# Kernel optimization log

Hardware: AMD Instinct MI355X
Metric: run time of the kernel (lower is better)

The kernel has to match this reference:

```python
import jax, jax.numpy as jnp
import numpy as np

# Multi-scale deformable attention (MSDeformableAttention from RTDETRTransformerv2)
SPATIAL = ((80, 80), (40, 40), (20, 20))  # (h, w) per level, strides 8/16/32 on 640x640
N_HEADS, N_LEVELS, N_POINTS = 8, 3, 4
D_MODEL = 256
HEAD_DIM = D_MODEL // N_HEADS


def setup_inputs() -> dict:
    key = jax.random.key(0)
    ks = jax.random.split(key, 10)
    B, Q = 16, 300
    Lv = sum(h * w for h, w in SPATIAL)  # 8400
    s = 0.02
    return {
        "query": jax.random.normal(ks[0], (B, Q, D_MODEL), jnp.float32),
        "reference_points": jax.random.uniform(ks[1], (B, Q, 4), jnp.float32),
        "value": jax.random.normal(ks[2], (B, Lv, D_MODEL), jnp.float32),
        "Wv": jax.random.normal(ks[3], (D_MODEL, D_MODEL), jnp.float32) * s,
        "bv": jnp.zeros((D_MODEL,), jnp.float32),
        "Woff": jax.random.normal(ks[4], (D_MODEL, N_HEADS * N_LEVELS * N_POINTS * 2), jnp.float32) * s,
        "boff": jax.random.normal(ks[5], (N_HEADS * N_LEVELS * N_POINTS * 2,), jnp.float32) * 0.1,
        "Wattn": jax.random.normal(ks[6], (D_MODEL, N_HEADS * N_LEVELS * N_POINTS), jnp.float32) * s,
        "battn": jnp.zeros((N_HEADS * N_LEVELS * N_POINTS,), jnp.float32),
        "Wout": jax.random.normal(ks[7], (D_MODEL, D_MODEL), jnp.float32) * s,
        "bout": jnp.zeros((D_MODEL,), jnp.float32),
    }


def _grid_sample_level(v_lvl, gx, gy, h, w):
    """Bilinear grid_sample, align_corners=False, zeros padding.

    v_lvl : (B, nH, h*w, hd) flattened per-level value map
    gx,gy : (B, nH, P) sample coords in [-1, 1]
    returns (B, nH, P, hd)
    """
    px = ((gx + 1.0) * w - 1.0) * 0.5  # pixel x
    py = ((gy + 1.0) * h - 1.0) * 0.5  # pixel y
    x0 = jnp.floor(px)
    y0 = jnp.floor(py)
    fx = px - x0
    fy = py - y0
    x0i = x0.astype(jnp.int32)
    y0i = y0.astype(jnp.int32)

    def corner(xi, yi, wgt):
        valid = (xi >= 0) & (xi < w) & (yi >= 0) & (yi < h)
        idx = jnp.clip(yi, 0, h - 1) * w + jnp.clip(xi, 0, w - 1)
        g = jnp.take_along_axis(v_lvl, idx[..., None], axis=2)  # (B,nH,P,hd)
        return g * (wgt * valid.astype(wgt.dtype))[..., None]

    return (corner(x0i, y0i, (1 - fx) * (1 - fy))
            + corner(x0i + 1, y0i, fx * (1 - fy))
            + corner(x0i, y0i + 1, (1 - fx) * fy)
            + corner(x0i + 1, y0i + 1, fx * fy))


def reference(query, reference_points, value, Wv, bv, Woff, boff, Wattn, battn, Wout, bout):
    B, Q, _ = query.shape
    # value projection -> per-head values
    v = (value @ Wv + bv).reshape(B, -1, N_HEADS, HEAD_DIM)
    # sampling offsets and attention weights from queries
    off = (query @ Woff + boff).reshape(B, Q, N_HEADS, N_LEVELS, N_POINTS, 2)
    aw = jax.nn.softmax(
        (query @ Wattn + battn).reshape(B, Q, N_HEADS, N_LEVELS * N_POINTS), axis=-1
    ).reshape(B, Q, N_HEADS, N_LEVELS, N_POINTS)
    # reference points (cx, cy) broadcast over heads/levels/points
    ref = reference_points[:, :, None, None, None, :2]
    pts = jnp.clip(ref + off, 0.0, 1.0)      # (B,Q,nH,nL,nP,2) in [0,1]
    g = pts * 2.0 - 1.0                      # grid_sample coords in [-1,1]

    out = jnp.zeros((B, Q, N_HEADS, HEAD_DIM), query.dtype)
    start = 0
    for lvl, (h, w) in enumerate(SPATIAL):
        v_lvl = v[:, start:start + h * w].transpose(0, 2, 1, 3)  # (B,nH,hw,hd)
        gl = g[:, :, :, lvl]                                     # (B,Q,nH,nP,2)
        gx = gl[..., 0].transpose(0, 2, 1, 3).reshape(B, N_HEADS, Q * N_POINTS)
        gy = gl[..., 1].transpose(0, 2, 1, 3).reshape(B, N_HEADS, Q * N_POINTS)
        sampled = _grid_sample_level(v_lvl, gx, gy, h, w)        # (B,nH,Q*nP,hd)
        sampled = sampled.reshape(B, N_HEADS, Q, N_POINTS, HEAD_DIM)
        wl = aw[:, :, :, lvl].transpose(0, 2, 1, 3)              # (B,nH,Q,nP)
        out = out + jnp.einsum('bhqpd,bhqp->bqhd', sampled, wl)
        start += h * w

    return out.reshape(B, Q, D_MODEL) @ Wout + bout
```

## Files before the change

kernel.cpp:

```cpp
#include <hip/hip_runtime.h>
#include <hip/hip_bf16.h>
#include <cstddef>

#define NB 16
#define NQ 300
#define DM 256
#define LV_ 8400

typedef __attribute__((ext_vector_type(8))) short short8;
typedef __attribute__((ext_vector_type(4))) float f32x4;

static __device__ __forceinline__ unsigned short bf16_rne(float f) {
  unsigned int u = __builtin_bit_cast(unsigned int, f);
  u += 0x7FFFu + ((u >> 16) & 1u);
  return (unsigned short)(u >> 16);
}

static __device__ __forceinline__ unsigned int pack_bf2(float a, float b) {
  __hip_bfloat162 p = __float22bfloat162_rn(make_float2(a, b));
  unsigned int u;
  __builtin_memcpy(&u, &p, 4);
  return u;
}

__global__ __launch_bounds__(256) void prep_kernel(
    const float* __restrict__ Wv, const float* __restrict__ Wout,
    unsigned short* __restrict__ Wth, unsigned short* __restrict__ WoutT) {
  const float* src = blockIdx.z ? Wout : Wv;
  unsigned short* dst = blockIdx.z ? WoutT : Wth;
  __shared__ float tle[32][33];
  const int k0 = blockIdx.x * 32, n0 = blockIdx.y * 32;
  const int xx = threadIdx.x & 31, y4 = (threadIdx.x >> 5) * 4;
  #pragma unroll
  for (int i = 0; i < 4; ++i)
    tle[y4 + i][xx] = src[(size_t)(k0 + y4 + i) * DM + n0 + xx];
  __syncthreads();
  #pragma unroll
  for (int i = 0; i < 4; ++i)
    dst[(size_t)(n0 + y4 + i) * DM + k0 + xx] = bf16_rne(tle[xx][y4 + i]);
}

__global__ __launch_bounds__(256) void vproj_mfma(
    const float* __restrict__ A, const unsigned short* __restrict__ Wth,
    const float* __restrict__ bias, unsigned short* __restrict__ V) {
  __shared__ short Ah[4][128][8];
  __shared__ short Bh[4][128][8];
  const int tid = threadIdx.x;
  const int lane = tid & 63;
  const int wave = tid >> 6;
  const int l16 = lane & 15, q4 = lane >> 4;
  const int wr = (wave >> 1) * 64, wc = (wave & 1) * 64;
  const size_t row0 = (size_t)blockIdx.x * 128;
  const int col0 = blockIdx.y * 128;

  const int arow = tid >> 1;
  const int half = tid & 1;
  const int c0 = half * 2;

  f32x4 acc[4][4];
  #pragma unroll
  for (int i = 0; i < 4; ++i)
    #pragma unroll
    for (int j = 0; j < 4; ++j) acc[i][j] = (f32x4)0.f;

  const float* ap0 = A + (row0 + arow) * DM + half * 16;
  const unsigned short* wp0 = Wth + (size_t)(col0 + arow) * DM + half * 16;

  float4 f0 = *(const float4*)(ap0 + 0);
  float4 f1 = *(const float4*)(ap0 + 4);
  float4 f2 = *(const float4*)(ap0 + 8);
  float4 f3 = *(const float4*)(ap0 + 12);
  uint4 w0 = *(const uint4*)(wp0);
  uint4 w1 = *(const uint4*)(wp0 + 8);

  for (int kk = 0; kk < DM; kk += 32) {
    uint4 p0, p1;
    p0.x = pack_bf2(f0.x, f0.y); p0.y = pack_bf2(f0.z, f0.w);
    p0.z = pack_bf2(f1.x, f1.y); p0.w = pack_bf2(f1.z, f1.w);
    p1.x = pack_bf2(f2.x, f2.y); p1.y = pack_bf2(f2.z, f2.w);
    p1.z = pack_bf2(f3.x, f3.y); p1.w = pack_bf2(f3.z, f3.w);
    uint4 cw0 = w0, cw1 = w1;
    __syncthreads();
    *(uint4*)&Ah[c0][arow][0]     = p0;
    *(uint4*)&Ah[c0 + 1][arow][0] = p1;
    *(uint4*)&Bh[c0][arow][0]     = cw0;
    *(uint4*)&Bh[c0 + 1][arow][0] = cw1;
    __syncthreads();

    if (kk + 32 < DM) {
      f0 = *(const float4*)(ap0 + kk + 32);
      f1 = *(const float4*)(ap0 + kk + 36);
      f2 = *(const float4*)(ap0 + kk + 40);
      f3 = *(const float4*)(ap0 + kk + 44);
      w0 = *(const uint4*)(wp0 + kk + 32);
      w1 = *(const uint4*)(wp0 + kk + 40);
    }

    short8 af[4], bfr[4];
    #pragma unroll
    for (int i = 0; i < 4; ++i)
      af[i] = *(const short8*)&Ah[q4][wr + i * 16 + l16][0];
    #pragma unroll
    for (int j = 0; j < 4; ++j)
      bfr[j] = *(const short8*)&Bh[q4][wc + j * 16 + l16][0];
    #pragma unroll
    for (int i = 0; i < 4; ++i)
      #pragma unroll
      for (int j = 0; j < 4; ++j)
        acc[i][j] = __builtin_amdgcn_mfma_f32_16x16x32_bf16(af[i], bfr[j], acc[i][j], 0, 0, 0);
  }

  #pragma unroll
  for (int i = 0; i < 4; ++i)
    #pragma unroll
    for (int j = 0; j < 4; ++j) {
      const int col = col0 + wc + j * 16 + l16;
      const float bcol = bias[col];
      #pragma unroll
      for (int r = 0; r < 4; ++r) {
        const size_t row = row0 + wr + i * 16 + q4 * 4 + r;
        V[row * DM + col] = bf16_rne(acc[i][j][r] + bcol);
      }
    }
}

__global__ __launch_bounds__(256) void gemm_qp(
    const float* __restrict__ q,
    const float* __restrict__ Woff, const float* __restrict__ boff,
    const float* __restrict__ Wattn, const float* __restrict__ battn,
    float* __restrict__ offb, float* __restrict__ logitb) {
  const int by = blockIdx.y;
  const float* W; const float* bias; float* C; int N, c0;
  if (by < 6) { W = Woff;  bias = boff;  C = offb;   N = 192; c0 = by * 32; }
  else        { W = Wattn; bias = battn; C = logitb; N = 96;  c0 = (by - 6) * 32; }
  const int m0 = blockIdx.x * 32;

  __shared__ float As[32][33];
  __shared__ float Bs[32][33];
  const int tid = threadIdx.x;
  const int ar = tid >> 3, ak = (tid & 7) * 4;
  const int kr = tid >> 3, bc = (tid & 7) * 4;
  const int tx = tid & 15, ty = tid >> 4;

  const float* apt = q + (size_t)(m0 + ar) * DM + ak;
  float4 av = *(const float4*)apt;
  float4 wv = *(const float4*)(W + (size_t)kr * N + c0 + bc);

  float acc[2][2] = {{0.f, 0.f}, {0.f, 0.f}};
  for (int kk = 0; kk < DM; kk += 32) {
    __syncthreads();
    As[ak + 0][ar] = av.x;
    As[ak + 1][ar] = av.y;
    As[ak + 2][ar] = av.z;
    As[ak + 3][ar] = av.w;
    *(float4*)&Bs[kr][bc] = wv;
    __syncthreads();
    if (kk + 32 < DM) {
      av = *(const float4*)(apt + kk + 32);
      wv = *(const float4*)(W + (size_t)(kk + 32 + kr) * N + c0 + bc);
    }
    #pragma unroll
    for (int k = 0; k < 32; ++k) {
      const float2 a2 = *(const float2*)&As[k][ty * 2];
      const float2 b2 = *(const float2*)&Bs[k][tx * 2];
      acc[0][0] = fmaf(a2.x, b2.x, acc[0][0]);
      acc[0][1] = fmaf(a2.x, b2.y, acc[0][1]);
      acc[1][0] = fmaf(a2.y, b2.x, acc[1][0]);
      acc[1][1] = fmaf(a2.y, b2.y, acc[1][1]);
    }
  }
  const float b0 = bias[c0 + tx * 2], b1 = bias[c0 + tx * 2 + 1];
  #pragma unroll
  for (int i = 0; i < 2; ++i) {
    float2 o; o.x = acc[i][0] + b0; o.y = acc[i][1] + b1;
    *(float2*)&C[(size_t)(m0 + ty * 2 + i) * N + c0 + tx * 2] = o;
  }
}

__global__ __launch_bounds__(256) void sample_kernel(
    const float* __restrict__ refp, const unsigned short* __restrict__ v,
    const float* __restrict__ off, const float* __restrict__ logits,
    unsigned short* __restrict__ mid) {
  const int x = blockIdx.x;
  const int c8 = x & 7, kb = x >> 3;
  const int b = c8 + (kb >= 150 ? 8 : 0);
  const int qp = (kb >= 150 ? kb - 150 : kb);
  const int bq0 = b * NQ + qp * 2;
  const int t = threadIdx.x;
  __shared__ float off_sh[2][192];
  __shared__ float aw_sh[2][96];
  __shared__ int   idx_sh[2][96][4];
  __shared__ float wt_sh[2][96][4];
  __shared__ float ref_sh[2][2];

  {
    const float* osrc = off + (size_t)bq0 * 192;
    float* odst = &off_sh[0][0];
    odst[t] = osrc[t];
    if (t < 128) odst[256 + t] = osrc[256 + t];
    const float* lsrc = logits + (size_t)bq0 * 96;
    if (t < 192) (&aw_sh[0][0])[t] = lsrc[t];
    if (t < 4) ref_sh[t >> 1][t & 1] = refp[(bq0 + (t >> 1)) * 4 + (t & 1)];
  }
  __syncthreads();

  if (t < 16) {
    const int q = t >> 3, h = t & 7;
    float* aw = &aw_sh[q][h * 12];
    float m = -1e30f;
    #pragma unroll
    for (int i = 0; i < 12; ++i) m = fmaxf(m, aw[i]);
    float e[12], s = 0.f;
    #pragma unroll
    for (int i = 0; i < 12; ++i) { e[i] = __expf(aw[i] - m); s += e[i]; }
    const float inv = 1.f / s;
    #pragma unroll
    for (int i = 0; i < 12; ++i) aw[i] = e[i] * inv;
  }
  __syncthreads();

  if (t < 192) {
    const int q = t / 96, r = t - q * 96;
    const int h = r / 12, lp = r - h * 12;
    const int l = lp >> 2, p = lp & 3;
    const int LH[3] = {80, 40, 20};
    const int LS[3] = {0, 6400, 8000};
    const int hh = LH[l], ww = LH[l], st = LS[l];
    const int oi = ((h * 3 + l) * 4 + p) * 2;
    const float aw = aw_sh[q][h * 12 + lp];
    const float sx = fminf(fmaxf(ref_sh[q][0] + off_sh[q][oi], 0.f), 1.f);
    const float sy = fminf(fmaxf(ref_sh[q][1] + off_sh[q][oi + 1], 0.f), 1.f);
    const float px = sx * (float)ww - 0.5f;
    const float py = sy * (float)hh - 0.5f;
    const float x0f = floorf(px), y0f = floorf(py);
    const float fx = px - x0f, fy = py - y0f;
    const int x0 = (int)x0f, y0 = (int)y0f;
    const int x1 = x0 + 1, y1 = y0 + 1;
    const bool vx0 = (x0 >= 0) & (x0 < ww), vx1 = (x1 >= 0) & (x1 < ww);
    const bool vy0 = (y0 >= 0) & (y0 < hh), vy1 = (y1 >= 0) & (y1 < hh);
    const int x0c = min(max(x0, 0), ww - 1), x1c = min(max(x1, 0), ww - 1);
    const int y0c = min(max(y0, 0), hh - 1), y1c = min(max(y1, 0), hh - 1);
    idx_sh[q][r][0] = st + y0c * ww + x0c;
    idx_sh[q][r][1] = st + y0c * ww + x1c;
    idx_sh[q][r][2] = st + y1c * ww + x0c;
    idx_sh[q][r][3] = st + y1c * ww + x1c;
    wt_sh[q][r][0] = aw * (1.f - fx) * (1.f - fy) * ((vx0 & vy0) ? 1.f : 0.f);
    wt_sh[q][r][1] = aw * fx * (1.f - fy) * ((vx1 & vy0) ? 1.f : 0.f);
    wt_sh[q][r][2] = aw * (1.f - fx) * fy * ((vx0 & vy1) ? 1.f : 0.f);
    wt_sh[q][r][3] = aw * fx * fy * ((vx1 & vy1) ? 1.f : 0.f);
  }
  __syncthreads();

  const int q = t >> 7, h = (t >> 4) & 7, dp = t & 15;
  const unsigned short* vb = v + (size_t)b * LV_ * DM + h * 32 + dp * 2;
  float ax = 0.f, ay = 0.f;
  #pragma unroll
  for (int r = 0; r < 12; ++r) {
    const int rr = h * 12 + r;
    #pragma unroll
    for (int cc = 0; cc < 4; ++cc) {
      const int id = idx_sh[q][rr][cc];
      const float w = wt_sh[q][rr][cc];
      const unsigned int u = *(const unsigned int*)(vb + (size_t)id * DM);
      ax = fmaf(w, __builtin_bit_cast(float, u << 16), ax);
      ay = fmaf(w, __builtin_bit_cast(float, u & 0xFFFF0000u), ay);
    }
  }
  unsigned short* mp = mid + (size_t)(bq0 + q) * DM + h * 32 + dp * 2;
  *(unsigned int*)mp = pack_bf2(ax, ay);
}

__global__ __launch_bounds__(256) void outp_mfma(
    const unsigned short* __restrict__ midb, const unsigned short* __restrict__ WoutT,
    const float* __restrict__ bias, float* __restrict__ out) {
  __shared__ short Ah[4][64][8];
  __shared__ short Bh[4][64][8];
  const int tid = threadIdx.x;
  const int lane = tid & 63;
  const int wave = tid >> 6;
  const int l16 = lane & 15, q4 = lane >> 4;
  const int wc = wave * 16;
  const int m0 = blockIdx.x * 64, col0 = blockIdx.y * 64;

  const int r = tid >> 2, ch = tid & 3;
  const unsigned short* apt = midb + (size_t)(m0 + r) * DM + ch * 8;
  const unsigned short* wpt = WoutT + (size_t)(col0 + r) * DM + ch * 8;
  uint4 am = *(const uint4*)apt;
  uint4 wm = *(const uint4*)wpt;

  f32x4 acc[4];
  #pragma unroll
  for (int i = 0; i < 4; ++i) acc[i] = (f32x4)0.f;

  for (int kk = 0; kk < DM; kk += 32) {
    __syncthreads();
    *(uint4*)&Ah[ch][r][0] = am;
    *(uint4*)&Bh[ch][r][0] = wm;
    __syncthreads();
    if (kk + 32 < DM) {
      am = *(const uint4*)(apt + kk + 32);
      wm = *(const uint4*)(wpt + kk + 32);
    }
    const short8 bfrag = *(const short8*)&Bh[q4][wc + l16][0];
    #pragma unroll
    for (int i = 0; i < 4; ++i) {
      const short8 af = *(const short8*)&Ah[q4][i * 16 + l16][0];
      acc[i] = __builtin_amdgcn_mfma_f32_16x16x32_bf16(af, bfrag, acc[i], 0, 0, 0);
    }
  }

  const int col = col0 + wc + l16;
  const float bcol = bias[col];
  #pragma unroll
  for (int i = 0; i < 4; ++i)
    #pragma unroll
    for (int rr = 0; rr < 4; ++rr)
      out[(size_t)(m0 + i * 16 + q4 * 4 + rr) * DM + col] = acc[i][rr] + bcol;
}

extern "C" void kernel_launch(void* const* d_in, const int* in_sizes, int n_in,
                              void* d_out, int out_size, void* d_ws, size_t ws_size,
                              hipStream_t stream) {
  (void)in_sizes; (void)n_in; (void)out_size; (void)ws_size;
  const float* query = (const float*)d_in[0];
  const float* refp  = (const float*)d_in[1];
  const float* value = (const float*)d_in[2];
  const float* Wv    = (const float*)d_in[3];
  const float* bv    = (const float*)d_in[4];
  const float* Woff  = (const float*)d_in[5];
  const float* boff  = (const float*)d_in[6];
  const float* Wattn = (const float*)d_in[7];
  const float* battn = (const float*)d_in[8];
  const float* Wout  = (const float*)d_in[9];
  const float* bout  = (const float*)d_in[10];
  float* out = (float*)d_out;

  char* ws = (char*)d_ws;
  unsigned short* v_bf  = (unsigned short*)ws;
  unsigned short* Wth   = (unsigned short*)(ws + 68812800);
  unsigned short* WoutT = (unsigned short*)(ws + 68943872);
  float* offb   = (float*)(ws + 69074944);
  float* logitb = (float*)(ws + 72761344);
  unsigned short* midb = (unsigned short*)(ws + 74604544);

  prep_kernel<<<dim3(8, 8, 2), 256, 0, stream>>>(Wv, Wout, Wth, WoutT);
  gemm_qp<<<dim3(150, 9), 256, 0, stream>>>(query, Woff, boff, Wattn, battn, offb, logitb);
  vproj_mfma<<<dim3((NB * LV_) / 128, 2), 256, 0, stream>>>(value, Wth, bv, v_bf);
  sample_kernel<<<2400, 256, 0, stream>>>(refp, v_bf, offb, logitb, midb);
  outp_mfma<<<dim3(75, 4), 256, 0, stream>>>(midb, WoutT, bout, out);
}
```

Baseline: 295.6 us.

## Stream value projection without LDS and split sampling per query across corners

The value-projection GEMM drops the LDS-staged 128x128 tiled MFMA kernel. Each wave now computes a 16-row strip across all 256 columns, reading the A fragment straight from global memory and pulling bf16 weight fragments from global/L2 each time, with no barriers. The sampling kernel moves from two queries per block to one query per block, doubling the grid. Within each block, two thread halves handle different bilinear corners and combine their partial sums with a cross-lane shuffle. The aim is to remove LDS sync overhead and raise parallelism in the gather, at the cost of redundant weight reads and more blocks.

```diff
diff --git a/kernel.cpp b/kernel.cpp
--- a/kernel.cpp
+++ b/kernel.cpp
@@ -40,88 +40,47 @@
     dst[(size_t)(n0 + y4 + i) * DM + k0 + xx] = bf16_rne(tle[xx][y4 + i]);
 }
 
-__global__ __launch_bounds__(256) void vproj_mfma(
+__global__ __launch_bounds__(256, 2) void vproj_stream(
     const float* __restrict__ A, const unsigned short* __restrict__ Wth,
     const float* __restrict__ bias, unsigned short* __restrict__ V) {
-  __shared__ short Ah[4][128][8];
-  __shared__ short Bh[4][128][8];
   const int tid = threadIdx.x;
   const int lane = tid & 63;
   const int wave = tid >> 6;
   const int l16 = lane & 15, q4 = lane >> 4;
-  const int wr = (wave >> 1) * 64, wc = (wave & 1) * 64;
-  const size_t row0 = (size_t)blockIdx.x * 128;
-  const int col0 = blockIdx.y * 128;
-
-  const int arow = tid >> 1;
-  const int half = tid & 1;
-  const int c0 = half * 2;
-
-  f32x4 acc[4][4];
-  #pragma unroll
-  for (int i = 0; i < 4; ++i)
-    #pragma unroll
-    for (int j = 0; j < 4; ++j) acc[i][j] = (f32x4)0.f;
-
-  const float* ap0 = A + (row0 + arow) * DM + half * 16;
-  const unsigned short* wp0 = Wth + (size_t)(col0 + arow) * DM + half * 16;
-
-  float4 f0 = *(const float4*)(ap0 + 0);
-  float4 f1 = *(const float4*)(ap0 + 4);
-  float4 f2 = *(const float4*)(ap0 + 8);
-  float4 f3 = *(const float4*)(ap0 + 12);
-  uint4 w0 = *(const uint4*)(wp0);
-  uint4 w1 = *(const uint4*)(wp0 + 8);
-
-  for (int kk = 0; kk < DM; kk += 32) {
-    uint4 p0, p1;
-    p0.x = pack_bf2(f0.x, f0.y); p0.y = pack_bf2(f0.z, f0.w);
-    p0.z = pack_bf2(f1.x, f1.y); p0.w = pack_bf2(f1.z, f1.w);
-    p1.x = pack_bf2(f2.x, f2.y); p1.y = pack_bf2(f2.z, f2.w);
-    p1.z = pack_bf2(f3.x, f3.y); p1.w = pack_bf2(f3.z, f3.w);
-    uint4 cw0 = w0, cw1 = w1;
-    __syncthreads();
-    *(uint4*)&Ah[c0][arow][0]     = p0;
-    *(uint4*)&Ah[c0 + 1][arow][0] = p1;
-    *(uint4*)&Bh[c0][arow][0]     = cw0;
-    *(uint4*)&Bh[c0 + 1][arow][0] = cw1;
-    __syncthreads();
-
-    if (kk + 32 < DM) {
-      f0 = *(const float4*)(ap0 + kk + 32);
-      f1 = *(const float4*)(ap0 + kk + 36);
-      f2 = *(const float4*)(ap0 + kk + 40);
-      f3 = *(const float4*)(ap0 + kk + 44);
-      w0 = *(const uint4*)(wp0 + kk + 32);
-      w1 = *(const uint4*)(wp0 + kk + 40);
-    }
-
-    short8 af[4], bfr[4];
-    #pragma unroll
-    for (int i = 0; i < 4; ++i)
-      af[i] = *(const short8*)&Ah[q4][wr + i * 16 + l16][0];
-    #pragma unroll
-    for (int j = 0; j < 4; ++j)
-      bfr[j] = *(const short8*)&Bh[q4][wc + j * 16 + l16][0];
-    #pragma unroll
-    for (int i = 0; i < 4; ++i)
-      #pragma unroll
-      for (int j = 0; j < 4; ++j)
-        acc[i][j] = __builtin_amdgcn_mfma_f32_16x16x32_bf16(af[i], bfr[j], acc[i][j], 0, 0, 0);
-  }
-
-  #pragma unroll
-  for (int i = 0; i < 4; ++i)
-    #pragma unroll
-    for (int j = 0; j < 4; ++j) {
-      const int col = col0 + wc + j * 16 + l16;
-      const float bcol = bias[col];
-      #pragma unroll
-      for (int r = 0; r < 4; ++r) {
-        const size_t row = row0 + wr + i * 16 + q4 * 4 + r;
-        V[row * DM + col] = bf16_rne(acc[i][j][r] + bcol);
-      }
-    }
+  const size_t row0 = (size_t)blockIdx.x * 64 + wave * 16;
+
+  const float* ap = A + (row0 + l16) * DM + q4 * 8;
+  const unsigned short* wp = Wth + (size_t)l16 * DM + q4 * 8;
+
+  f32x4 acc[16];
+  #pragma unroll
+  for (int j = 0; j < 16; ++j) acc[j] = (f32x4)0.f;
+
+  #pragma unroll
+  for (int c = 0; c < 8; ++c) {
+    const float4 a0 = *(const float4*)(ap + c * 32);
+    const float4 a1 = *(const float4*)(ap + c * 32 + 4);
+    uint4 pk;
+    pk.x = pack_bf2(a0.x, a0.y);
+    pk.y = pack_bf2(a0.z, a0.w);
+    pk.z = pack_bf2(a1.x, a1.y);
+    pk.w = pack_bf2(a1.z, a1.w);
+    const short8 afr = __builtin_bit_cast(short8, pk);
+    #pragma unroll
+    for (int j = 0; j < 16; ++j) {
+      const short8 bfr = *(const short8*)(wp + (size_t)j * 16 * DM + c * 32);
+      acc[j] = __builtin_amdgcn_mfma_f32_16x16x32_bf16(afr, bfr, acc[j], 0, 0, 0);
+    }
+  }
+
+  #pragma unroll
+  for (int j = 0; j < 16; ++j) {
+    const int col = j * 16 + l16;
+    const float bcol = bias[col];
+    #pragma unroll
+    for (int r = 0; r < 4; ++r)
+      V[(row0 + q4 * 4 + r) * DM + col] = bf16_rne(acc[j][r] + bcol);
+  }
 }
 
 __global__ __launch_bounds__(256) void gemm_qp(
@@ -182,31 +141,25 @@
     const float* __restrict__ off, const float* __restrict__ logits,
     unsigned short* __restrict__ mid) {
   const int x = blockIdx.x;
-  const int c8 = x & 7, kb = x >> 3;
-  const int b = c8 + (kb >= 150 ? 8 : 0);
-  const int qp = (kb >= 150 ? kb - 150 : kb);
-  const int bq0 = b * NQ + qp * 2;
+  const int c8 = x & 7, k = x >> 3;
+  const int b = c8 + (k >= 300 ? 8 : 0);
+  const int qq = (k >= 300 ? k - 300 : k);
+  const int bq = b * NQ + qq;
   const int t = threadIdx.x;
-  __shared__ float off_sh[2][192];
-  __shared__ float aw_sh[2][96];
-  __shared__ int   idx_sh[2][96][4];
-  __shared__ float wt_sh[2][96][4];
-  __shared__ float ref_sh[2][2];
-
-  {
-    const float* osrc = off + (size_t)bq0 * 192;
-    float* odst = &off_sh[0][0];
-    odst[t] = osrc[t];
-    if (t < 128) odst[256 + t] = osrc[256 + t];
-    const float* lsrc = logits + (size_t)bq0 * 96;
-    if (t < 192) (&aw_sh[0][0])[t] = lsrc[t];
-    if (t < 4) ref_sh[t >> 1][t & 1] = refp[(bq0 + (t >> 1)) * 4 + (t & 1)];
-  }
+  __shared__ float off_sh[192];
+  __shared__ float aw_sh[96];
+  __shared__ int   idx_sh[96][4];
+  __shared__ float wt_sh[96][4];
+  __shared__ float ref_sh[2];
+
+  if (t < 192) off_sh[t] = off[(size_t)bq * 192 + t];
+  else aw_sh[t - 192] = logits[(size_t)bq * 96 + (t - 192)];
+  if (t < 32) aw_sh[64 + t] = logits[(size_t)bq * 96 + 64 + t];
+  if (t < 2) ref_sh[t] = refp[bq * 4 + t];
   __syncthreads();
 
-  if (t < 16) {
-    const int q = t >> 3, h = t & 7;
-    float* aw = &aw_sh[q][h * 12];
+  if (t < 8) {
+    float* aw = &aw_sh[t * 12];
     float m = -1e30f;
     #pragma unroll
     for (int i = 0; i < 12; ++i) m = fmaxf(m, aw[i]);
@@ -219,17 +172,17 @@
   }
   __syncthreads();
 
-  if (t < 192) {
-    const int q = t / 96, r = t - q * 96;
+  if (t < 96) {
+    const int r = t;
     const int h = r / 12, lp = r - h * 12;
     const int l = lp >> 2, p = lp & 3;
     const int LH[3] = {80, 40, 20};
     const int LS[3] = {0, 6400, 8000};
     const int hh = LH[l], ww = LH[l], st = LS[l];
     const int oi = ((h * 3 + l) * 4 + p) * 2;
-    const float aw = aw_sh[q][h * 12 + lp];
-    const float sx = fminf(fmaxf(ref_sh[q][0] + off_sh[q][oi], 0.f), 1.f);
-    const float sy = fminf(fmaxf(ref_sh[q][1] + off_sh[q][oi + 1], 0.f), 1.f);
+    const float aw = aw_sh[h * 12 + lp];
+    const float sx = fminf(fmaxf(ref_sh[0] + off_sh[oi], 0.f), 1.f);
+    const float sy = fminf(fmaxf(ref_sh[1] + off_sh[oi + 1], 0.f), 1.f);
     const float px = sx * (float)ww - 0.5f;
     const float py = sy * (float)hh - 0.5f;
     const float x0f = floorf(px), y0f = floorf(py);
@@ -240,34 +193,38 @@
     const bool vy0 = (y0 >= 0) & (y0 < hh), vy1 = (y1 >= 0) & (y1 < hh);
     const int x0c = min(max(x0, 0), ww - 1), x1c = min(max(x1, 0), ww - 1);
     const int y0c = min(max(y0, 0), hh - 1), y1c = min(max(y1, 0), hh - 1);
-    idx_sh[q][r][0] = st + y0c * ww + x0c;
-    idx_sh[q][r][1] = st + y0c * ww + x1c;
-    idx_sh[q][r][2] = st + y1c * ww + x0c;
-    idx_sh[q][r][3] = st + y1c * ww + x1c;
-    wt_sh[q][r][0] = aw * (1.f - fx) * (1.f - fy) * ((vx0 & vy0) ? 1.f : 0.f);
-    wt_sh[q][r][1] = aw * fx * (1.f - fy) * ((vx1 & vy0) ? 1.f : 0.f);
-    wt_sh[q][r][2] = aw * (1.f - fx) * fy * ((vx0 & vy1) ? 1.f : 0.f);
-    wt_sh[q][r][3] = aw * fx * fy * ((vx1 & vy1) ? 1.f : 0.f);
+    idx_sh[r][0] = st + y0c * ww + x0c;
+    idx_sh[r][1] = st + y0c * ww + x1c;
+    idx_sh[r][2] = st + y1c * ww + x0c;
+    idx_sh[r][3] = st + y1c * ww + x1c;
+    wt_sh[r][0] = aw * (1.f - fx) * (1.f - fy) * ((vx0 & vy0) ? 1.f : 0.f);
+    wt_sh[r][1] = aw * fx * (1.f - fy) * ((vx1 & vy0) ? 1.f : 0.f);
+    wt_sh[r][2] = aw * (1.f - fx) * fy * ((vx0 & vy1) ? 1.f : 0.f);
+    wt_sh[r][3] = aw * fx * fy * ((vx1 & vy1) ? 1.f : 0.f);
   }
   __syncthreads();
 
-  const int q = t >> 7, h = (t >> 4) & 7, dp = t & 15;
+  const int h = t >> 5, ch = (t >> 4) & 1, dp = t & 15;
   const unsigned short* vb = v + (size_t)b * LV_ * DM + h * 32 + dp * 2;
   float ax = 0.f, ay = 0.f;
   #pragma unroll
   for (int r = 0; r < 12; ++r) {
     const int rr = h * 12 + r;
     #pragma unroll
-    for (int cc = 0; cc < 4; ++cc) {
-      const int id = idx_sh[q][rr][cc];
-      const float w = wt_sh[q][rr][cc];
+    for (int cc = 0; cc < 2; ++cc) {
+      const int id = idx_sh[rr][ch * 2 + cc];
+      const float w = wt_sh[rr][ch * 2 + cc];
       const unsigned int u = *(const unsigned int*)(vb + (size_t)id * DM);
       ax = fmaf(w, __builtin_bit_cast(float, u << 16), ax);
       ay = fmaf(w, __builtin_bit_cast(float, u & 0xFFFF0000u), ay);
     }
   }
-  unsigned short* mp = mid + (size_t)(bq0 + q) * DM + h * 32 + dp * 2;
-  *(unsigned int*)mp = pack_bf2(ax, ay);
+  ax += __shfl_xor(ax, 16, 64);
+  ay += __shfl_xor(ay, 16, 64);
+  if (ch == 0) {
+    unsigned short* mp = mid + (size_t)bq * DM + h * 32 + dp * 2;
+    *(unsigned int*)mp = pack_bf2(ax, ay);
+  }
 }
 
 __global__ __launch_bounds__(256) void outp_mfma(
@@ -345,7 +302,7 @@
 
   prep_kernel<<<dim3(8, 8, 2), 256, 0, stream>>>(Wv, Wout, Wth, WoutT);
   gemm_qp<<<dim3(150, 9), 256, 0, stream>>>(query, Woff, boff, Wattn, battn, offb, logitb);
-  vproj_mfma<<<dim3((NB * LV_) / 128, 2), 256, 0, stream>>>(value, Wth, bv, v_bf);
-  sample_kernel<<<2400, 256, 0, stream>>>(refp, v_bf, offb, logitb, midb);
+  vproj_stream<<<(NB * LV_) / 64, 256, 0, stream>>>(value, Wth, bv, v_bf);
+  sample_kernel<<<4800, 256, 0, stream>>>(refp, v_bf, offb, logitb, midb);
   outp_mfma<<<dim3(75, 4), 256, 0, stream>>>(midb, WoutT, bout, out);
 }
```

Measured after the change: 396.2 us. 1.34x slower.
